# Kernel tuning notes

Hardware: AMD Instinct MI355X
Metric: run time of the kernel (lower is better)

Reference implementation:

```python
import jax, jax.numpy as jnp
import numpy as np
import math

D_MODEL = 1024
HEAD_DIM = 64
B, T = 4, 4096


def setup_inputs() -> dict:
    key = jax.random.key(0)
    kx, kq, kk, kv = jax.random.split(key, 4)
    s = 1.0 / math.sqrt(D_MODEL)  # torch Linear default init scale (approx, uniform->normal ok for ref)
    return {
        "x": jax.random.normal(kx, (B, T, D_MODEL), dtype=jnp.float32),
        "Wq": jax.random.normal(kq, (HEAD_DIM, D_MODEL), dtype=jnp.float32) * s,
        "Wk": jax.random.normal(kk, (HEAD_DIM, D_MODEL), dtype=jnp.float32) * s,
        "Wv": jax.random.normal(kv, (HEAD_DIM, D_MODEL), dtype=jnp.float32) * s,
        "energy": jnp.asarray(1.0, dtype=jnp.float32),
    }


def reference(x, Wq, Wk, Wv, energy):
    # Projections: nn.Linear(d_model, head_dim, bias=False) -> x @ W.T
    q = jnp.einsum("btc,hc->bth", x, Wq)  # [B,T,H]
    k = jnp.einsum("btc,hc->bth", x, Wk)
    v = jnp.einsum("btc,hc->bth", x, Wv)

    scale = 1.0 / math.sqrt(HEAD_DIM)
    scores = jnp.einsum("bqh,bkh->bqk", q, k) * scale  # [B,T,T]
    attn = jax.nn.softmax(scores, axis=-1)
    out = jnp.einsum("bqk,bkh->bqh", attn, v)  # [B,T,H]

    # Entropy of attention rows, averaged over batch and queries
    attn_entropy = -jnp.sum(attn * jnp.log(attn + 1e-8), axis=-1).mean()
    # Metabolic EMA side-effect (stateful in torch; returned here for completeness)
    new_energy = 0.9 * energy + 0.1 * attn_entropy

    return out, attn, new_energy
```

## Files before the change

### kernel.cpp

```cpp
#include <hip/hip_runtime.h>

#define PITCH 72
#define PPITCH 68

typedef __attribute__((ext_vector_type(8))) short bf16x8;
typedef __attribute__((ext_vector_type(4))) float f32x4;
typedef __attribute__((ext_vector_type(8))) unsigned short u16x8;

__device__ __forceinline__ unsigned short f2bf(float f) {
  union { float f; unsigned int u; } v; v.f = f;
  unsigned int u = v.u + 0x7fffu + ((v.u >> 16) & 1u);
  return (unsigned short)(u >> 16);
}

__device__ __forceinline__ f32x4 mfma16(bf16x8 a, bf16x8 b, f32x4 c) {
  return __builtin_amdgcn_mfma_f32_16x16x32_bf16(a, b, c, 0, 0, 0);
}

__global__ __launch_bounds__(256) void qkv_kernel(
    const float* __restrict__ x, const float* __restrict__ Wq,
    const float* __restrict__ Wk, const float* __restrict__ Wv,
    unsigned short* __restrict__ q_ws, unsigned short* __restrict__ k_ws,
    unsigned short* __restrict__ vT_ws) {
  __shared__ unsigned short Xs[64 * PITCH];
  __shared__ unsigned short Ws[64 * PITCH];

  const int tid = threadIdx.x;
  const int wave = tid >> 6, lane = tid & 63;
  const int quad = lane >> 4, l16 = lane & 15;
  const int bx = blockIdx.x;
  const int mt = bx / 3, which = bx - mt * 3;
  const int m0 = mt * 64;
  const float* wp = (which == 0) ? Wq : ((which == 1) ? Wk : Wv);

  f32x4 acc[4];
#pragma unroll
  for (int i = 0; i < 4; ++i) acc[i] = (f32x4)0.0f;

  const int srow = tid >> 4, sc4 = tid & 15;
  for (int k0 = 0; k0 < 1024; k0 += 64) {
#pragma unroll
    for (int i = 0; i < 4; ++i) {
      int row = srow + i * 16;
      float4 f = *(const float4*)(x + (size_t)(m0 + row) * 1024 + k0 + sc4 * 4);
      *(ushort4*)&Xs[row * PITCH + sc4 * 4] =
          make_ushort4(f2bf(f.x), f2bf(f.y), f2bf(f.z), f2bf(f.w));
      float4 g = *(const float4*)(wp + (size_t)row * 1024 + k0 + sc4 * 4);
      *(ushort4*)&Ws[row * PITCH + sc4 * 4] =
          make_ushort4(f2bf(g.x), f2bf(g.y), f2bf(g.z), f2bf(g.w));
    }
    __syncthreads();
#pragma unroll
    for (int ks = 0; ks < 64; ks += 32) {
      bf16x8 a = *(const bf16x8*)&Xs[(wave * 16 + l16) * PITCH + ks + quad * 8];
#pragma unroll
      for (int nt = 0; nt < 4; ++nt) {
        bf16x8 b = *(const bf16x8*)&Ws[(nt * 16 + l16) * PITCH + ks + quad * 8];
        acc[nt] = mfma16(a, b, acc[nt]);
      }
    }
    __syncthreads();
  }

  const int mrow = wave * 16 + quad * 4;
  if (which == 0) {
#pragma unroll
    for (int nt = 0; nt < 4; ++nt)
#pragma unroll
      for (int r = 0; r < 4; ++r)
        q_ws[(size_t)(m0 + mrow + r) * 64 + nt * 16 + l16] = f2bf(acc[nt][r] * 0.125f);
  } else if (which == 1) {
#pragma unroll
    for (int nt = 0; nt < 4; ++nt)
#pragma unroll
      for (int r = 0; r < 4; ++r)
        k_ws[(size_t)(m0 + mrow + r) * 64 + nt * 16 + l16] = f2bf(acc[nt][r]);
  } else {
#pragma unroll
    for (int nt = 0; nt < 4; ++nt)
#pragma unroll
      for (int r = 0; r < 4; ++r)
        Xs[(nt * 16 + l16) * PITCH + mrow + r] = f2bf(acc[nt + 0][r]);
    __syncthreads();
    const int b = m0 >> 12, t0 = m0 & 4095;
#pragma unroll
    for (int i = 0; i < 2; ++i) {
      int cc = tid + i * 256;
      int h = cc >> 3, c8 = cc & 7;
      u16x8 v = *(const u16x8*)&Xs[h * PITCH + c8 * 8];
      *(u16x8*)(vT_ws + ((size_t)b * 64 + h) * 4096 + t0 + c8 * 8) = v;
    }
  }
}

__global__ __launch_bounds__(256) void flash_kernel(
    const unsigned short* __restrict__ q_ws, const unsigned short* __restrict__ k_ws,
    const unsigned short* __restrict__ vT_ws, float* __restrict__ Opart,
    float* __restrict__ Spart, float* __restrict__ Wpart) {
  __shared__ unsigned short Qs[64 * PITCH];
  __shared__ unsigned short Ks[64 * PITCH];
  __shared__ unsigned short Vts[64 * PITCH];
  __shared__ unsigned short Ps[4][16 * PPITCH];

  const int tid = threadIdx.x;
  const int wave = tid >> 6, lane = tid & 63;
  const int quad = lane >> 4, l16 = lane & 15;
  const int bx = blockIdx.x;
  const int ksp = bx & 3, qt = (bx >> 2) & 63, b = bx >> 8;
  const int q0 = qt * 64;

  const unsigned short* qb = q_ws + ((size_t)b * 4096 + q0) * 64;
  const unsigned short* kb = k_ws + (size_t)b * 4096 * 64;
  const unsigned short* vtb = vT_ws + (size_t)b * 64 * 4096;

#pragma unroll
  for (int i = 0; i < 2; ++i) {
    int cc = tid + i * 256;
    int row = cc >> 3, c8 = cc & 7;
    *(u16x8*)&Qs[row * PITCH + c8 * 8] = *(const u16x8*)(qb + (size_t)row * 64 + c8 * 8);
  }

  f32x4 Oacc[4];
#pragma unroll
  for (int i = 0; i < 4; ++i) Oacc[i] = (f32x4)0.0f;
  float sumE[4] = {0.f, 0.f, 0.f, 0.f};
  float sumES[4] = {0.f, 0.f, 0.f, 0.f};

  __syncthreads();

  for (int kt = ksp * 16; kt < ksp * 16 + 16; ++kt) {
    const int k0 = kt * 64;
#pragma unroll
    for (int i = 0; i < 2; ++i) {
      int cc = tid + i * 256;
      int row = cc >> 3, c8 = cc & 7;
      *(u16x8*)&Ks[row * PITCH + c8 * 8] =
          *(const u16x8*)(kb + (size_t)(k0 + row) * 64 + c8 * 8);
      *(u16x8*)&Vts[row * PITCH + c8 * 8] =
          *(const u16x8*)(vtb + (size_t)row * 4096 + k0 + c8 * 8);
    }
    __syncthreads();

    f32x4 s[4];
#pragma unroll
    for (int i = 0; i < 4; ++i) s[i] = (f32x4)0.0f;
#pragma unroll
    for (int ks = 0; ks < 64; ks += 32) {
      bf16x8 a = *(const bf16x8*)&Qs[(wave * 16 + l16) * PITCH + ks + quad * 8];
#pragma unroll
      for (int nt = 0; nt < 4; ++nt) {
        bf16x8 bk = *(const bf16x8*)&Ks[(nt * 16 + l16) * PITCH + ks + quad * 8];
        s[nt] = mfma16(a, bk, s[nt]);
      }
    }
#pragma unroll
    for (int nt = 0; nt < 4; ++nt)
#pragma unroll
      for (int r = 0; r < 4; ++r) {
        float sv = s[nt][r];
        float e = __expf(sv);
        sumE[r] += e;
        sumES[r] += e * sv;
        Ps[wave][(quad * 4 + r) * PPITCH + nt * 16 + l16] = f2bf(e);
      }
#pragma unroll
    for (int kk = 0; kk < 64; kk += 32) {
      bf16x8 a = *(const bf16x8*)&Ps[wave][l16 * PPITCH + kk + quad * 8];
#pragma unroll
      for (int ht = 0; ht < 4; ++ht) {
        bf16x8 bv = *(const bf16x8*)&Vts[(ht * 16 + l16) * PITCH + kk + quad * 8];
        Oacc[ht] = mfma16(a, bv, Oacc[ht]);
      }
    }
    __syncthreads();
  }

#pragma unroll
  for (int off = 1; off < 16; off <<= 1)
#pragma unroll
    for (int r = 0; r < 4; ++r) {
      sumE[r] += __shfl_xor(sumE[r], off, 64);
      sumES[r] += __shfl_xor(sumES[r], off, 64);
    }
  const int mrow = wave * 16 + quad * 4;
  if (l16 == 0)
#pragma unroll
    for (int r = 0; r < 4; ++r) {
      Spart[(size_t)bx * 64 + mrow + r] = sumE[r];
      Wpart[(size_t)bx * 64 + mrow + r] = sumES[r];
    }
  float* Op = Opart + (size_t)bx * 4096;
#pragma unroll
  for (int ht = 0; ht < 4; ++ht)
#pragma unroll
    for (int r = 0; r < 4; ++r)
      Op[(size_t)(mrow + r) * 64 + ht * 16 + l16] = Oacc[ht][r];
}

__global__ __launch_bounds__(256) void combine_kernel(
    const float* __restrict__ Opart, const float* __restrict__ Spart,
    const float* __restrict__ Wpart, float* __restrict__ out,
    float* __restrict__ invS, float* __restrict__ entAcc) {
  __shared__ float invLds[64];
  const int tid = threadIdx.x;
  const int bx = blockIdx.x;

  if (tid < 64) {
    float S = 0.f, W = 0.f;
#pragma unroll
    for (int ks = 0; ks < 4; ++ks) {
      S += Spart[(size_t)(bx * 4 + ks) * 64 + tid];
      W += Wpart[(size_t)(bx * 4 + ks) * 64 + tid];
    }
    float inv = 1.0f / S;
    invS[(size_t)bx * 64 + tid] = inv;
    invLds[tid] = inv;
    float ent = __logf(S) - W * inv;
#pragma unroll
    for (int off = 1; off < 64; off <<= 1) ent += __shfl_xor(ent, off, 64);
    if (tid == 0) atomicAdd(entAcc, ent);
  }
  __syncthreads();

  const int r = tid >> 2, cg = tid & 3;
  float inv = invLds[r];
#pragma unroll
  for (int j = 0; j < 4; ++j) {
    int c = cg * 16 + j * 4;
    f32x4 s = (f32x4)0.0f;
#pragma unroll
    for (int ks = 0; ks < 4; ++ks)
      s += *(const f32x4*)(Opart + (size_t)(bx * 4 + ks) * 4096 + r * 64 + c);
    s *= inv;
    *(f32x4*)(out + ((size_t)bx * 64 + r) * 64 + c) = s;
  }
}

__global__ __launch_bounds__(256) void attn_write_kernel(
    const unsigned short* __restrict__ q_ws, const unsigned short* __restrict__ k_ws,
    const float* __restrict__ invS, float* __restrict__ attn) {
  __shared__ unsigned short Qs[64 * PITCH];
  __shared__ unsigned short Ks[128 * PITCH];
  __shared__ float invLds[64];

  const int tid = threadIdx.x;
  const int wave = tid >> 6, lane = tid & 63;
  const int quad = lane >> 4, l16 = lane & 15;
  const int bx = blockIdx.x;
  const int kc = bx & 31, qt = (bx >> 5) & 63, b = bx >> 11;
  const int q0 = qt * 64, k0g = kc * 128;

  const unsigned short* qb = q_ws + ((size_t)b * 4096 + q0) * 64;
  const unsigned short* kb = k_ws + ((size_t)b * 4096 + k0g) * 64;

#pragma unroll
  for (int i = 0; i < 2; ++i) {
    int cc = tid + i * 256;
    int row = cc >> 3, c8 = cc & 7;
    *(u16x8*)&Qs[row * PITCH + c8 * 8] = *(const u16x8*)(qb + (size_t)row * 64 + c8 * 8);
  }
#pragma unroll
  for (int i = 0; i < 4; ++i) {
    int cc = tid + i * 256;
    int row = cc >> 3, c8 = cc & 7;
    *(u16x8*)&Ks[row * PITCH + c8 * 8] = *(const u16x8*)(kb + (size_t)row * 64 + c8 * 8);
  }
  if (tid < 64) invLds[tid] = invS[(size_t)(b * 64 + qt) * 64 + tid];
  __syncthreads();

  f32x4 s[8];
#pragma unroll
  for (int i = 0; i < 8; ++i) s[i] = (f32x4)0.0f;
#pragma unroll
  for (int ks = 0; ks < 64; ks += 32) {
    bf16x8 a = *(const bf16x8*)&Qs[(wave * 16 + l16) * PITCH + ks + quad * 8];
#pragma unroll
    for (int nt = 0; nt < 8; ++nt) {
      bf16x8 bk = *(const bf16x8*)&Ks[(nt * 16 + l16) * PITCH + ks + quad * 8];
      s[nt] = mfma16(a, bk, s[nt]);
    }
  }

  float invR[4];
#pragma unroll
  for (int r = 0; r < 4; ++r) invR[r] = invLds[wave * 16 + quad * 4 + r];

  float* ab = attn + (size_t)b * 4096 * 4096;
#pragma unroll
  for (int nt = 0; nt < 8; ++nt)
#pragma unroll
    for (int r = 0; r < 4; ++r) {
      int m = q0 + wave * 16 + quad * 4 + r;
      ab[(size_t)m * 4096 + k0g + nt * 16 + l16] = __expf(s[nt][r]) * invR[r];
    }
}

__global__ void energy_kernel(const float* __restrict__ energy,
                              const float* __restrict__ entAcc,
                              float* __restrict__ dst) {
  if (threadIdx.x == 0 && blockIdx.x == 0)
    dst[0] = 0.9f * energy[0] + 0.1f * (entAcc[0] * (1.0f / 16384.0f));
}

extern "C" void kernel_launch(void* const* d_in, const int* in_sizes, int n_in,
                              void* d_out, int out_size, void* d_ws, size_t ws_size,
                              hipStream_t stream) {
  (void)in_sizes; (void)n_in; (void)out_size; (void)ws_size;
  const float* x = (const float*)d_in[0];
  const float* Wq = (const float*)d_in[1];
  const float* Wk = (const float*)d_in[2];
  const float* Wv = (const float*)d_in[3];
  const float* energy = (const float*)d_in[4];

  float* out = (float*)d_out;
  float* attn = out + (size_t)4 * 4096 * 64;
  float* dst_energy = attn + (size_t)4 * 4096 * 4096;

  char* ws = (char*)d_ws;
  float* entAcc = (float*)ws;
  unsigned short* q_ws = (unsigned short*)(ws + 256);
  unsigned short* k_ws = q_ws + (size_t)16384 * 64;
  unsigned short* vT_ws = k_ws + (size_t)16384 * 64;
  float* invS = (float*)(vT_ws + (size_t)16384 * 64);
  float* Spart = invS + 16384;
  float* Wpart = Spart + 1024 * 64;
  float* Opart = Wpart + 1024 * 64;

  hipMemsetAsync(entAcc, 0, sizeof(float), stream);
  qkv_kernel<<<768, 256, 0, stream>>>(x, Wq, Wk, Wv, q_ws, k_ws, vT_ws);
  flash_kernel<<<1024, 256, 0, stream>>>(q_ws, k_ws, vT_ws, Opart, Spart, Wpart);
  combine_kernel<<<256, 256, 0, stream>>>(Opart, Spart, Wpart, out, invS, entAcc);
  attn_write_kernel<<<8192, 256, 0, stream>>>(q_ws, k_ws, invS, attn);
  energy_kernel<<<1, 64, 0, stream>>>(energy, entAcc, dst_energy);
}
```

Baseline: 437.2 us.

## Stage attention tile through LDS for vectorized nontemporal stores; XCD-aware QKV block mapping

The attention-write kernel now writes the normalized probability tile into an LDS buffer that aliases the Q/K staging area. It then reads it back as float4 rows, so the 256 MB attn matrix is written with 16-byte nontemporal stores instead of scattered 4-byte stores. The QKV projection kernel remaps block indices so blocks sharing an x tile land on the same XCD for L2 reuse. The cost is two extra barriers and an LDS round trip per tile.

```diff
diff --git a/kernel.cpp b/kernel.cpp
--- a/kernel.cpp
+++ b/kernel.cpp
@@ -2,6 +2,7 @@
 
 #define PITCH 72
 #define PPITCH 68
+#define APITCH 132
 
 typedef __attribute__((ext_vector_type(8))) short bf16x8;
 typedef __attribute__((ext_vector_type(4))) float f32x4;
@@ -29,7 +30,9 @@
   const int wave = tid >> 6, lane = tid & 63;
   const int quad = lane >> 4, l16 = lane & 15;
   const int bx = blockIdx.x;
-  const int mt = bx / 3, which = bx - mt * 3;
+  const int xcd = bx & 7, rr = bx >> 3;
+  const int g = rr / 3, which = rr - g * 3;
+  const int mt = (g << 3) + xcd;
   const int m0 = mt * 64;
   const float* wp = (which == 0) ? Wq : ((which == 1) ? Wk : Wv);
 
@@ -45,9 +48,9 @@
       float4 f = *(const float4*)(x + (size_t)(m0 + row) * 1024 + k0 + sc4 * 4);
       *(ushort4*)&Xs[row * PITCH + sc4 * 4] =
           make_ushort4(f2bf(f.x), f2bf(f.y), f2bf(f.z), f2bf(f.w));
-      float4 g = *(const float4*)(wp + (size_t)row * 1024 + k0 + sc4 * 4);
+      float4 gg = *(const float4*)(wp + (size_t)row * 1024 + k0 + sc4 * 4);
       *(ushort4*)&Ws[row * PITCH + sc4 * 4] =
-          make_ushort4(f2bf(g.x), f2bf(g.y), f2bf(g.z), f2bf(g.w));
+          make_ushort4(f2bf(gg.x), f2bf(gg.y), f2bf(gg.z), f2bf(gg.w));
     }
     __syncthreads();
 #pragma unroll
@@ -239,9 +242,11 @@
 __global__ __launch_bounds__(256) void attn_write_kernel(
     const unsigned short* __restrict__ q_ws, const unsigned short* __restrict__ k_ws,
     const float* __restrict__ invS, float* __restrict__ attn) {
-  __shared__ unsigned short Qs[64 * PITCH];
-  __shared__ unsigned short Ks[128 * PITCH];
+  __shared__ __align__(16) char ldsbuf[64 * APITCH * 4];
   __shared__ float invLds[64];
+  unsigned short* Qs = (unsigned short*)ldsbuf;
+  unsigned short* Ks = (unsigned short*)(ldsbuf + 64 * PITCH * 2);
+  float* As = (float*)ldsbuf;
 
   const int tid = threadIdx.x;
   const int wave = tid >> 6, lane = tid & 63;
@@ -285,14 +290,30 @@
 #pragma unroll
   for (int r = 0; r < 4; ++r) invR[r] = invLds[wave * 16 + quad * 4 + r];
 
-  float* ab = attn + (size_t)b * 4096 * 4096;
 #pragma unroll
   for (int nt = 0; nt < 8; ++nt)
 #pragma unroll
-    for (int r = 0; r < 4; ++r) {
-      int m = q0 + wave * 16 + quad * 4 + r;
-      ab[(size_t)m * 4096 + k0g + nt * 16 + l16] = __expf(s[nt][r]) * invR[r];
-    }
+    for (int r = 0; r < 4; ++r) s[nt][r] = __expf(s[nt][r]) * invR[r];
+
+  __syncthreads();
+
+  const int arow = wave * 16 + quad * 4;
+#pragma unroll
+  for (int nt = 0; nt < 8; ++nt)
+#pragma unroll
+    for (int r = 0; r < 4; ++r)
+      As[(arow + r) * APITCH + nt * 16 + l16] = s[nt][r];
+
+  __syncthreads();
+
+  float* ab = attn + (size_t)b * 4096 * 4096 + (size_t)q0 * 4096 + k0g;
+#pragma unroll
+  for (int j = 0; j < 8; ++j) {
+    int idx = tid + j * 256;
+    int row = idx >> 5, c = idx & 31;
+    f32x4 v = *(const f32x4*)&As[row * APITCH + c * 4];
+    __builtin_nontemporal_store(v, (f32x4*)(ab + (size_t)row * 4096 + c * 4));
+  }
 }
 
 __global__ void energy_kernel(const float* __restrict__ energy,
```

After: 432.6 us. Within noise of the previous version (-1.1%).

## Fuse flash, combine and attention-write into one persistent kernel per query tile

Applied to the files above, without the earlier changes.

Replaces the split-K flash kernel, the combine kernel and the separate attention-write kernel with one 512-thread kernel per 64-query tile. Two wave groups split the keys, reduce sums and outputs through shared memory, then recompute the scores to write normalised attention with nontemporal stores. K and V are read straight from global memory instead of being staged in shared memory, and block indices are remapped so tiles land on chiplet (XCD) groups. This removes the partial-buffer round trips and two launches, but only 256 blocks run, each doing a long serial loop, so occupancy and latency hiding may suffer.

```diff
diff --git a/kernel.cpp b/kernel.cpp
--- a/kernel.cpp
+++ b/kernel.cpp
@@ -2,6 +2,7 @@
 
 #define PITCH 72
 #define PPITCH 68
+#define OSPITCH 68
 
 typedef __attribute__((ext_vector_type(8))) short bf16x8;
 typedef __attribute__((ext_vector_type(4))) float f32x4;
@@ -29,7 +30,9 @@
   const int wave = tid >> 6, lane = tid & 63;
   const int quad = lane >> 4, l16 = lane & 15;
   const int bx = blockIdx.x;
-  const int mt = bx / 3, which = bx - mt * 3;
+  const int xcd = bx & 7, rr = bx >> 3;
+  const int g = rr / 3, which = rr - g * 3;
+  const int mt = (g << 3) + xcd;
   const int m0 = mt * 64;
   const float* wp = (which == 0) ? Wq : ((which == 1) ? Wk : Wv);
 
@@ -45,9 +48,9 @@
       float4 f = *(const float4*)(x + (size_t)(m0 + row) * 1024 + k0 + sc4 * 4);
       *(ushort4*)&Xs[row * PITCH + sc4 * 4] =
           make_ushort4(f2bf(f.x), f2bf(f.y), f2bf(f.z), f2bf(f.w));
-      float4 g = *(const float4*)(wp + (size_t)row * 1024 + k0 + sc4 * 4);
+      float4 gg = *(const float4*)(wp + (size_t)row * 1024 + k0 + sc4 * 4);
       *(ushort4*)&Ws[row * PITCH + sc4 * 4] =
-          make_ushort4(f2bf(g.x), f2bf(g.y), f2bf(g.z), f2bf(g.w));
+          make_ushort4(f2bf(gg.x), f2bf(gg.y), f2bf(gg.z), f2bf(gg.w));
     }
     __syncthreads();
 #pragma unroll
@@ -93,32 +96,31 @@
   }
 }
 
-__global__ __launch_bounds__(256) void flash_kernel(
+__global__ __launch_bounds__(512) void fused_kernel(
     const unsigned short* __restrict__ q_ws, const unsigned short* __restrict__ k_ws,
-    const unsigned short* __restrict__ vT_ws, float* __restrict__ Opart,
-    float* __restrict__ Spart, float* __restrict__ Wpart) {
-  __shared__ unsigned short Qs[64 * PITCH];
-  __shared__ unsigned short Ks[64 * PITCH];
-  __shared__ unsigned short Vts[64 * PITCH];
-  __shared__ unsigned short Ps[4][16 * PPITCH];
+    const unsigned short* __restrict__ vT_ws, float* __restrict__ out,
+    float* __restrict__ attn, float* __restrict__ entAcc) {
+  __shared__ unsigned short Ps[8][16 * PPITCH];
+  __shared__ float redE[2][64], redES[2][64];
+  __shared__ float invLds[64];
 
   const int tid = threadIdx.x;
   const int wave = tid >> 6, lane = tid & 63;
   const int quad = lane >> 4, l16 = lane & 15;
+  const int qs = wave & 3, kh = wave >> 2;
   const int bx = blockIdx.x;
-  const int ksp = bx & 3, qt = (bx >> 2) & 63, b = bx >> 8;
+  const int xcd = bx & 7, j = bx >> 3;
+  const int b = xcd >> 1, qt = (xcd & 1) * 32 + j;
   const int q0 = qt * 64;
 
   const unsigned short* qb = q_ws + ((size_t)b * 4096 + q0) * 64;
   const unsigned short* kb = k_ws + (size_t)b * 4096 * 64;
   const unsigned short* vtb = vT_ws + (size_t)b * 64 * 4096;
 
-#pragma unroll
-  for (int i = 0; i < 2; ++i) {
-    int cc = tid + i * 256;
-    int row = cc >> 3, c8 = cc & 7;
-    *(u16x8*)&Qs[row * PITCH + c8 * 8] = *(const u16x8*)(qb + (size_t)row * 64 + c8 * 8);
-  }
+  bf16x8 aq[2];
+#pragma unroll
+  for (int ks = 0; ks < 2; ++ks)
+    aq[ks] = *(const bf16x8*)(qb + (size_t)(qs * 16 + l16) * 64 + ks * 32 + quad * 8);
 
   f32x4 Oacc[4];
 #pragma unroll
@@ -126,33 +128,19 @@
   float sumE[4] = {0.f, 0.f, 0.f, 0.f};
   float sumES[4] = {0.f, 0.f, 0.f, 0.f};
 
-  __syncthreads();
-
-  for (int kt = ksp * 16; kt < ksp * 16 + 16; ++kt) {
-    const int k0 = kt * 64;
-#pragma unroll
-    for (int i = 0; i < 2; ++i) {
-      int cc = tid + i * 256;
-      int row = cc >> 3, c8 = cc & 7;
-      *(u16x8*)&Ks[row * PITCH + c8 * 8] =
-          *(const u16x8*)(kb + (size_t)(k0 + row) * 64 + c8 * 8);
-      *(u16x8*)&Vts[row * PITCH + c8 * 8] =
-          *(const u16x8*)(vtb + (size_t)row * 4096 + k0 + c8 * 8);
-    }
-    __syncthreads();
-
+  for (int it = 0; it < 32; ++it) {
+    const int k0 = it * 128 + kh * 64;
     f32x4 s[4];
 #pragma unroll
     for (int i = 0; i < 4; ++i) s[i] = (f32x4)0.0f;
 #pragma unroll
-    for (int ks = 0; ks < 64; ks += 32) {
-      bf16x8 a = *(const bf16x8*)&Qs[(wave * 16 + l16) * PITCH + ks + quad * 8];
+    for (int ks = 0; ks < 2; ++ks)
 #pragma unroll
       for (int nt = 0; nt < 4; ++nt) {
-        bf16x8 bk = *(const bf16x8*)&Ks[(nt * 16 + l16) * PITCH + ks + quad * 8];
-        s[nt] = mfma16(a, bk, s[nt]);
-      }
-    }
+        bf16x8 bk = *(const bf16x8*)(kb + (size_t)(k0 + nt * 16 + l16) * 64 +
+                                     ks * 32 + quad * 8);
+        s[nt] = mfma16(aq[ks], bk, s[nt]);
+      }
 #pragma unroll
     for (int nt = 0; nt < 4; ++nt)
 #pragma unroll
@@ -164,15 +152,15 @@
         Ps[wave][(quad * 4 + r) * PPITCH + nt * 16 + l16] = f2bf(e);
       }
 #pragma unroll
-    for (int kk = 0; kk < 64; kk += 32) {
-      bf16x8 a = *(const bf16x8*)&Ps[wave][l16 * PPITCH + kk + quad * 8];
+    for (int kk = 0; kk < 2; ++kk) {
+      bf16x8 a = *(const bf16x8*)&Ps[wave][l16 * PPITCH + kk * 32 + quad * 8];
 #pragma unroll
       for (int ht = 0; ht < 4; ++ht) {
-        bf16x8 bv = *(const bf16x8*)&Vts[(ht * 16 + l16) * PITCH + kk + quad * 8];
+        bf16x8 bv = *(const bf16x8*)(vtb + (size_t)(ht * 16 + l16) * 4096 + k0 +
+                                     kk * 32 + quad * 8);
         Oacc[ht] = mfma16(a, bv, Oacc[ht]);
       }
     }
-    __syncthreads();
   }
 
 #pragma unroll
@@ -182,38 +170,27 @@
       sumE[r] += __shfl_xor(sumE[r], off, 64);
       sumES[r] += __shfl_xor(sumES[r], off, 64);
     }
-  const int mrow = wave * 16 + quad * 4;
+  const int mrow = qs * 16 + quad * 4;
   if (l16 == 0)
 #pragma unroll
     for (int r = 0; r < 4; ++r) {
-      Spart[(size_t)bx * 64 + mrow + r] = sumE[r];
-      Wpart[(size_t)bx * 64 + mrow + r] = sumES[r];
-    }
-  float* Op = Opart + (size_t)bx * 4096;
-#pragma unroll
-  for (int ht = 0; ht < 4; ++ht)
-#pragma unroll
-    for (int r = 0; r < 4; ++r)
-      Op[(size_t)(mrow + r) * 64 + ht * 16 + l16] = Oacc[ht][r];
-}
-
-__global__ __launch_bounds__(256) void combine_kernel(
-    const float* __restrict__ Opart, const float* __restrict__ Spart,
-    const float* __restrict__ Wpart, float* __restrict__ out,
-    float* __restrict__ invS, float* __restrict__ entAcc) {
-  __shared__ float invLds[64];
-  const int tid = threadIdx.x;
-  const int bx = blockIdx.x;
-
+      redE[kh][mrow + r] = sumE[r];
+      redES[kh][mrow + r] = sumES[r];
+    }
+  __syncthreads();
+
+  float* Osum = (float*)&Ps[0][0];
+  if (kh == 1) {
+#pragma unroll
+    for (int ht = 0; ht < 4; ++ht)
+#pragma unroll
+      for (int r = 0; r < 4; ++r)
+        Osum[(mrow + r) * OSPITCH + ht * 16 + l16] = Oacc[ht][r];
+  }
   if (tid < 64) {
-    float S = 0.f, W = 0.f;
-#pragma unroll
-    for (int ks = 0; ks < 4; ++ks) {
-      S += Spart[(size_t)(bx * 4 + ks) * 64 + tid];
-      W += Wpart[(size_t)(bx * 4 + ks) * 64 + tid];
-    }
+    float S = redE[0][tid] + redE[1][tid];
+    float W = redES[0][tid] + redES[1][tid];
     float inv = 1.0f / S;
-    invS[(size_t)bx * 64 + tid] = inv;
     invLds[tid] = inv;
     float ent = __logf(S) - W * inv;
 #pragma unroll
@@ -222,77 +199,43 @@
   }
   __syncthreads();
 
-  const int r = tid >> 2, cg = tid & 3;
-  float inv = invLds[r];
-#pragma unroll
-  for (int j = 0; j < 4; ++j) {
-    int c = cg * 16 + j * 4;
-    f32x4 s = (f32x4)0.0f;
-#pragma unroll
-    for (int ks = 0; ks < 4; ++ks)
-      s += *(const f32x4*)(Opart + (size_t)(bx * 4 + ks) * 4096 + r * 64 + c);
-    s *= inv;
-    *(f32x4*)(out + ((size_t)bx * 64 + r) * 64 + c) = s;
-  }
-}
-
-__global__ __launch_bounds__(256) void attn_write_kernel(
-    const unsigned short* __restrict__ q_ws, const unsigned short* __restrict__ k_ws,
-    const float* __restrict__ invS, float* __restrict__ attn) {
-  __shared__ unsigned short Qs[64 * PITCH];
-  __shared__ unsigned short Ks[128 * PITCH];
-  __shared__ float invLds[64];
-
-  const int tid = threadIdx.x;
-  const int wave = tid >> 6, lane = tid & 63;
-  const int quad = lane >> 4, l16 = lane & 15;
-  const int bx = blockIdx.x;
-  const int kc = bx & 31, qt = (bx >> 5) & 63, b = bx >> 11;
-  const int q0 = qt * 64, k0g = kc * 128;
-
-  const unsigned short* qb = q_ws + ((size_t)b * 4096 + q0) * 64;
-  const unsigned short* kb = k_ws + ((size_t)b * 4096 + k0g) * 64;
-
-#pragma unroll
-  for (int i = 0; i < 2; ++i) {
-    int cc = tid + i * 256;
-    int row = cc >> 3, c8 = cc & 7;
-    *(u16x8*)&Qs[row * PITCH + c8 * 8] = *(const u16x8*)(qb + (size_t)row * 64 + c8 * 8);
-  }
-#pragma unroll
-  for (int i = 0; i < 4; ++i) {
-    int cc = tid + i * 256;
-    int row = cc >> 3, c8 = cc & 7;
-    *(u16x8*)&Ks[row * PITCH + c8 * 8] = *(const u16x8*)(kb + (size_t)row * 64 + c8 * 8);
-  }
-  if (tid < 64) invLds[tid] = invS[(size_t)(b * 64 + qt) * 64 + tid];
-  __syncthreads();
-
-  f32x4 s[8];
-#pragma unroll
-  for (int i = 0; i < 8; ++i) s[i] = (f32x4)0.0f;
-#pragma unroll
-  for (int ks = 0; ks < 64; ks += 32) {
-    bf16x8 a = *(const bf16x8*)&Qs[(wave * 16 + l16) * PITCH + ks + quad * 8];
-#pragma unroll
-    for (int nt = 0; nt < 8; ++nt) {
-      bf16x8 bk = *(const bf16x8*)&Ks[(nt * 16 + l16) * PITCH + ks + quad * 8];
-      s[nt] = mfma16(a, bk, s[nt]);
-    }
+  if (kh == 0) {
+#pragma unroll
+    for (int ht = 0; ht < 4; ++ht)
+#pragma unroll
+      for (int r = 0; r < 4; ++r) {
+        float o = Oacc[ht][r] + Osum[(mrow + r) * OSPITCH + ht * 16 + l16];
+        out[((size_t)b * 4096 + q0 + mrow + r) * 64 + ht * 16 + l16] =
+            o * invLds[mrow + r];
+      }
   }
 
   float invR[4];
 #pragma unroll
-  for (int r = 0; r < 4; ++r) invR[r] = invLds[wave * 16 + quad * 4 + r];
-
-  float* ab = attn + (size_t)b * 4096 * 4096;
-#pragma unroll
-  for (int nt = 0; nt < 8; ++nt)
-#pragma unroll
-    for (int r = 0; r < 4; ++r) {
-      int m = q0 + wave * 16 + quad * 4 + r;
-      ab[(size_t)m * 4096 + k0g + nt * 16 + l16] = __expf(s[nt][r]) * invR[r];
-    }
+  for (int r = 0; r < 4; ++r) invR[r] = invLds[mrow + r];
+
+  float* ab = attn + ((size_t)b * 4096 + q0 + qs * 16) * 4096;
+  for (int it = 0; it < 32; ++it) {
+    const int k0 = it * 128 + kh * 64;
+    f32x4 s[4];
+#pragma unroll
+    for (int i = 0; i < 4; ++i) s[i] = (f32x4)0.0f;
+#pragma unroll
+    for (int ks = 0; ks < 2; ++ks)
+#pragma unroll
+      for (int nt = 0; nt < 4; ++nt) {
+        bf16x8 bk = *(const bf16x8*)(kb + (size_t)(k0 + nt * 16 + l16) * 64 +
+                                     ks * 32 + quad * 8);
+        s[nt] = mfma16(aq[ks], bk, s[nt]);
+      }
+#pragma unroll
+    for (int nt = 0; nt < 4; ++nt)
+#pragma unroll
+      for (int r = 0; r < 4; ++r)
+        __builtin_nontemporal_store(
+            __expf(s[nt][r]) * invR[r],
+            ab + (size_t)(quad * 4 + r) * 4096 + k0 + nt * 16 + l16);
+  }
 }
 
 __global__ void energy_kernel(const float* __restrict__ energy,
@@ -321,15 +264,9 @@
   unsigned short* q_ws = (unsigned short*)(ws + 256);
   unsigned short* k_ws = q_ws + (size_t)16384 * 64;
   unsigned short* vT_ws = k_ws + (size_t)16384 * 64;
-  float* invS = (float*)(vT_ws + (size_t)16384 * 64);
-  float* Spart = invS + 16384;
-  float* Wpart = Spart + 1024 * 64;
-  float* Opart = Wpart + 1024 * 64;
 
   hipMemsetAsync(entAcc, 0, sizeof(float), stream);
   qkv_kernel<<<768, 256, 0, stream>>>(x, Wq, Wk, Wv, q_ws, k_ws, vT_ws);
-  flash_kernel<<<1024, 256, 0, stream>>>(q_ws, k_ws, vT_ws, Opart, Spart, Wpart);
-  combine_kernel<<<256, 256, 0, stream>>>(Opart, Spart, Wpart, out, invS, entAcc);
-  attn_write_kernel<<<8192, 256, 0, stream>>>(q_ws, k_ws, invS, attn);
+  fused_kernel<<<256, 512, 0, stream>>>(q_ws, k_ws, vT_ws, out, attn, entAcc);
   energy_kernel<<<1, 64, 0, stream>>>(energy, entAcc, dst_energy);
 }
```

Measured after the change: 516.3 us. +18.1%, slower.
